# Kernel optimization log

Hardware: AMD Instinct MI355X
Metric: run time of the kernel (lower is better)

## Reference

```python
import jax, jax.numpy as jnp
import numpy as np
from jax import lax

THRESHOLD = 0.7
OUT = 224  # output size of nn.Upsample(size=(224,224), mode='bilinear', align_corners=True)


def _bilinear(img, xs, ys):
    """align_corners=True bilinear sampling. img: (..., H, W); xs: (oh,), ys: (ow,) float coords."""
    H, W = img.shape[-2], img.shape[-1]
    x0 = jnp.clip(jnp.floor(xs).astype(jnp.int32), 0, H - 1)
    x1 = jnp.clip(x0 + 1, 0, H - 1)
    y0 = jnp.clip(jnp.floor(ys).astype(jnp.int32), 0, W - 1)
    y1 = jnp.clip(y0 + 1, 0, W - 1)
    wx = (xs - x0.astype(xs.dtype))[:, None]  # (oh,1)
    wy = (ys - y0.astype(ys.dtype))[None, :]  # (1,ow)
    top = jnp.take(img, x0, axis=-2)
    bot = jnp.take(img, x1, axis=-2)
    v00 = jnp.take(top, y0, axis=-1)
    v01 = jnp.take(top, y1, axis=-1)
    v10 = jnp.take(bot, y0, axis=-1)
    v11 = jnp.take(bot, y1, axis=-1)
    return (1 - wx) * ((1 - wy) * v00 + wy * v01) + wx * ((1 - wy) * v10 + wy * v11)


def _normalize01(h):
    n = h.shape[0]
    f = h.reshape(n, -1)
    mn = f.min(axis=1, keepdims=True)
    mx = f.max(axis=1, keepdims=True)
    return ((f - mn) / (mx - mn)).reshape(h.shape)


def _largest_cc(mask):
    """8-connected (skimage connectivity=2) largest component via min-label propagation.
    mask: (N,H,W) bool -> (N,H,W) bool, True on the largest connected component."""
    N, H, W = mask.shape
    BIG = H * W  # background sentinel label
    idx = jnp.arange(BIG, dtype=jnp.int32).reshape(1, H, W)
    lab0 = jnp.where(mask, idx, BIG)

    def body(state):
        lab, _ = state
        pooled = lax.reduce_window(lab, jnp.int32(BIG), lax.min, (1, 3, 3), (1, 1, 1), 'SAME')
        new = jnp.where(mask, pooled, BIG)
        return new, jnp.any(new != lab)

    lab, _ = lax.while_loop(lambda s: s[1], body, (lab0, jnp.bool_(True)))

    def counts(l):
        return jnp.zeros(BIG + 1, jnp.int32).at[l.reshape(-1)].add(1)

    c = jax.vmap(counts)(lab)                 # (N, H*W+1); last bin = background
    best = jnp.argmax(c[:, :BIG], axis=1)     # label of largest foreground component
    return lab == best[:, None, None]


def _bbox(lcc):
    N, H, W = lcc.shape
    rows = lcc.any(axis=2)
    cols = lcc.any(axis=1)
    has = rows.any(axis=1)
    xmin = jnp.argmax(rows, axis=1).astype(jnp.int32)
    xmax = (H - 1 - jnp.argmax(rows[:, ::-1], axis=1)).astype(jnp.int32)
    ymin = jnp.argmax(cols, axis=1).astype(jnp.int32)
    ymax = (W - 1 - jnp.argmax(cols[:, ::-1], axis=1)).astype(jnp.int32)
    # fallback to full image if the mask is empty (torch code would crash here)
    xmin = jnp.where(has, xmin, 0)
    ymin = jnp.where(has, ymin, 0)
    xmax = jnp.where(has, xmax, H - 1)
    ymax = jnp.where(has, ymax, W - 1)
    return xmin, xmax, ymin, ymax


def _crop_resize(images, xmin, xmax, ymin, ymax):
    # torch crop is images[i][:, xmin:xmax, ymin:ymax] (exclusive upper), then align_corners resize
    grid = jnp.arange(OUT, dtype=jnp.float32) / (OUT - 1)

    def one(img, a, b, c, d):
        Lx = jnp.maximum(b - a, 1)
        Ly = jnp.maximum(d - c, 1)
        xs = a.astype(jnp.float32) + grid * (Lx - 1).astype(jnp.float32)
        ys = c.astype(jnp.float32) + grid * (Ly - 1).astype(jnp.float32)
        return _bilinear(img, xs, ys)

    return jax.vmap(one)(images, xmin, xmax, ymin, ymax)


def setup_inputs() -> dict:
    key = jax.random.key(0)
    k1, k2 = jax.random.split(key)
    x = jax.random.normal(k1, (64, 3, 224, 224), dtype=jnp.float32)
    features = jax.random.normal(k2, (64, 2048, 7, 7), dtype=jnp.float32)
    return {"x": x, "features": features}


def reference(x, features):
    # distance = normalize01(Lmax(features, axis=1))
    heat = _normalize01(jnp.max(jnp.abs(features), axis=1))       # (N, h, w)
    h, w = heat.shape[1], heat.shape[2]
    grid = jnp.arange(OUT, dtype=jnp.float32) / (OUT - 1)
    out_heatmap = _bilinear(heat, grid * (h - 1), grid * (w - 1))  # (N, 224, 224)
    mask = out_heatmap > THRESHOLD
    lcc = _largest_cc(mask)
    xmin, xmax, ymin, ymax = _bbox(lcc)
    crop = _crop_resize(x, xmin, xmax, ymin, ymax)                 # (N, 3, 224, 224)
    coords = jnp.stack([ymin, xmin, ymax, xmax], axis=1)           # (N, 4), torch coord order
    return crop, out_heatmap, coords
```

## Files before the change

### kernel.cpp

```cpp
#include <hip/hip_runtime.h>
#include <stdint.h>

#define NIMG   64
#define NCH    2048
#define HW7    49
#define OUTW   224
#define NPIX   50176
#define CROP_N 9633792
#define HEAT_OFF  9633792
#define COORD_OFF 12845056
#define THRESH 0.7f

#define MAXR 8
#define RCAP (224*MAXR)
#define NWORDS 784
#define WPAD   788

#define SCRATCH_ULL 52480

__global__ __launch_bounds__(256) void k0_zero(unsigned long long* base) {
    int id = blockIdx.x * 256 + threadIdx.x;
    if (id < SCRATCH_ULL) base[id] = 0ull;
}

__global__ __launch_bounds__(256) void k1_heat(const float* __restrict__ F,
                                               unsigned* __restrict__ heatBins) {
    __shared__ unsigned hU[HW7];
    const int t = threadIdx.x;
    const int b = blockIdx.x;
    const int n = b >> 3, chunk = b & 7;
    if (t < HW7) hU[t] = 0u;
    __syncthreads();
    const float* Fp = F + (size_t)n * 100352 + (size_t)chunk * 12544 + t;
    int pos = t % 49;
#pragma unroll
    for (int r = 0; r < 49; ++r) {
        float v = fabsf(Fp[r * 256]);
        atomicMax(&hU[pos], __float_as_uint(v));
        pos += 11; if (pos >= 49) pos -= 49;
    }
    __syncthreads();
    if (t < HW7) atomicMax(&heatBins[n * HW7 + t], hU[t]);
}

__device__ inline float bilin7(const float* h7, int i, int j) {
#pragma clang fp contract(off)
    float gx = (float)i / 223.0f;
    float gy = (float)j / 223.0f;
    float xs = gx * 6.0f;
    float ys = gy * 6.0f;
    int x0 = (int)floorf(xs); x0 = min(max(x0, 0), 6); int x1 = min(x0 + 1, 6);
    int y0 = (int)floorf(ys); y0 = min(max(y0, 0), 6); int y1 = min(y0 + 1, 6);
    float wx = xs - (float)x0;
    float wy = ys - (float)y0;
    float v00 = h7[x0 * 7 + y0], v01 = h7[x0 * 7 + y1];
    float v10 = h7[x1 * 7 + y0], v11 = h7[x1 * 7 + y1];
    return (1.0f - wx) * ((1.0f - wy) * v00 + wy * v01)
         + wx * ((1.0f - wy) * v10 + wy * v11);
}

__global__ __launch_bounds__(256) void k2_heatmap(const unsigned* __restrict__ heatBins,
                                                  float* __restrict__ heatOut,
                                                  unsigned long long* __restrict__ maskW) {
    __shared__ float raw[HW7];
    __shared__ float h7[HW7];
    __shared__ float s_mn, s_mx;
    const int t = threadIdx.x;
    const int b = blockIdx.x;
    const int n = b >> 3, slice = b & 7;
    if (t < HW7) raw[t] = __uint_as_float(heatBins[n * HW7 + t]);
    __syncthreads();
    if (t == 0) {
        float mn = raw[0], mx = raw[0];
        for (int i = 1; i < HW7; ++i) { float v = raw[i]; mn = fminf(mn, v); mx = fmaxf(mx, v); }
        s_mn = mn; s_mx = mx;
    }
    __syncthreads();
    if (t < HW7) h7[t] = (raw[t] - s_mn) / (s_mx - s_mn);
    __syncthreads();

    const int pbase = slice * 6272;
    for (int k = 0; k < 25; ++k) {
        int pl = k * 256 + t;
        if (pl < 6272) {
            int p = pbase + pl;
            int i = p / 224, j = p % 224;
            float val = bilin7(h7, i, j);
            heatOut[(size_t)n * NPIX + p] = val;
            unsigned long long bal = __ballot(val > THRESH);
            if ((t & 63) == 0) maskW[(size_t)n * WPAD + (p >> 6)] = bal;
        }
    }
}

__device__ inline unsigned uf_find(volatile unsigned* P, unsigned x) {
    while (true) {
        unsigned p = P[x];
        if (p == x) return x;
        unsigned gp = P[p];
        if (gp == p) return p;
        P[x] = gp;
        x = gp;
    }
}

__device__ inline void uf_merge(volatile unsigned* P, unsigned a, unsigned b) {
    while (true) {
        a = uf_find(P, a); b = uf_find(P, b);
        if (a == b) return;
        if (a > b) { unsigned tmp = a; a = b; b = tmp; }
        unsigned old = atomicCAS((unsigned*)&P[b], b, a);
        if (old == b) return;
        b = old;
    }
}

__global__ __launch_bounds__(256) void k3_ccl(const unsigned long long* __restrict__ maskW,
                                              float* __restrict__ coords) {
    __shared__ unsigned long long W[WPAD];
    __shared__ unsigned short runS[RCAP], runE[RCAP];
    __shared__ unsigned char nRuns[224];
    __shared__ unsigned parent[RCAP], cnt[RCAP];
    __shared__ unsigned rmin[RCAP], rmax[RCAP], cmin[RCAP], cmax[RCAP];
    __shared__ unsigned bestScore, bestRid;
    const int t = threadIdx.x;
    const int n = blockIdx.x;

    for (int i = t; i < WPAD; i += 256) W[i] = maskW[(size_t)n * WPAD + i];
    for (int i = t; i < RCAP; i += 256) {
        parent[i] = (unsigned)i; cnt[i] = 0u;
        rmin[i] = 0xFFFFFFFFu; rmax[i] = 0u; cmin[i] = 0xFFFFFFFFu; cmax[i] = 0u;
    }
    if (t == 0) { bestScore = 0u; bestRid = 0u; }
    __syncthreads();

    if (t < 224) {
        const int r = t;
        const int bit0 = r * 224;
        const int w0 = bit0 >> 6, sh = bit0 & 63;
        unsigned long long rb[4];
#pragma unroll
        for (int q = 0; q < 4; ++q) {
            unsigned long long lo = W[w0 + q] >> sh;
            unsigned long long hi = sh ? (W[w0 + q + 1] << (64 - sh)) : 0ull;
            rb[q] = lo | hi;
        }
        rb[3] &= 0xFFFFFFFFull;

        unsigned long long st[4], en[4];
        unsigned long long carry = 0ull;
#pragma unroll
        for (int q = 0; q < 4; ++q) {
            unsigned long long shl = (rb[q] << 1) | carry;
            carry = rb[q] >> 63;
            st[q] = rb[q] & ~shl;
        }
#pragma unroll
        for (int q = 0; q < 4; ++q) {
            unsigned long long nxt = (q < 3) ? rb[q + 1] : 0ull;
            en[q] = rb[q] & ~((rb[q] >> 1) | (nxt << 63));
        }
        int ns = 0;
#pragma unroll
        for (int q = 0; q < 4; ++q) {
            unsigned long long x = st[q];
            while (x) {
                int z = __builtin_ctzll(x); x &= x - 1;
                if (ns < MAXR) runS[r * MAXR + ns] = (unsigned short)(q * 64 + z);
                ns++;
            }
        }
        int ne = 0;
#pragma unroll
        for (int q = 0; q < 4; ++q) {
            unsigned long long x = en[q];
            while (x) {
                int z = __builtin_ctzll(x); x &= x - 1;
                if (ne < MAXR) runE[r * MAXR + ne] = (unsigned short)(q * 64 + z);
                ne++;
            }
        }
        nRuns[r] = (unsigned char)min(ns, MAXR);
    }
    __syncthreads();

    if (t >= 1 && t < 224) {
        const int r = t;
        const int na = nRuns[r], nb = nRuns[r - 1];
        for (int k = 0; k < na; ++k) {
            int rid = r * MAXR + k;
            int s = runS[rid], e = runE[rid];
            for (int m = 0; m < nb; ++m) {
                int qid = (r - 1) * MAXR + m;
                int s2 = runS[qid], e2 = runE[qid];
                if (s2 <= e + 1 && e2 >= s - 1) uf_merge(parent, (unsigned)rid, (unsigned)qid);
            }
        }
    }
    __syncthreads();

    for (int rid = t; rid < RCAP; rid += 256) {
        int r = rid >> 3, k = rid & (MAXR - 1);
        if (k < (int)nRuns[r]) {
            int s = runS[rid], e = runE[rid];
            unsigned root = uf_find(parent, (unsigned)rid);
            atomicAdd(&cnt[root], (unsigned)(e - s + 1));
            atomicMin(&rmin[root], (unsigned)r);
            atomicMax(&rmax[root], (unsigned)r);
            atomicMin(&cmin[root], (unsigned)s);
            atomicMax(&cmax[root], (unsigned)e);
        }
    }
    __syncthreads();

    for (int rid = t; rid < RCAP; rid += 256) {
        unsigned c = cnt[rid];
        if (c > 0u) {
            unsigned label = (unsigned)((rid >> 3) * 224 + (int)runS[rid]);
            unsigned score = (c << 16) | (65535u - label);
            atomicMax(&bestScore, score);
        }
    }
    __syncthreads();
    for (int rid = t; rid < RCAP; rid += 256) {
        unsigned c = cnt[rid];
        if (c > 0u) {
            unsigned label = (unsigned)((rid >> 3) * 224 + (int)runS[rid]);
            unsigned score = (c << 16) | (65535u - label);
            if (score == bestScore) bestRid = (unsigned)rid;
        }
    }
    __syncthreads();

    if (t == 0) {
        int xmin, xmax, ymin, ymax;
        if (bestScore == 0u) {
            xmin = 0; ymin = 0; xmax = 223; ymax = 223;
        } else {
            unsigned rb_ = bestRid;
            xmin = (int)rmin[rb_]; xmax = (int)rmax[rb_];
            ymin = (int)cmin[rb_]; ymax = (int)cmax[rb_];
        }
        coords[n * 4 + 0] = (float)ymin;
        coords[n * 4 + 1] = (float)xmin;
        coords[n * 4 + 2] = (float)ymax;
        coords[n * 4 + 3] = (float)xmax;
    }
}

__global__ __launch_bounds__(256) void k4_crop(const float* __restrict__ X,
                                               const float* __restrict__ coords,
                                               float* __restrict__ out) {
#pragma clang fp contract(off)
    int id = blockIdx.x * 256 + threadIdx.x;
    if (id >= CROP_N) return;
    int n   = id / 150528;
    int rem = id % 150528;
    int p   = rem % NPIX;
    int oi  = p / 224, oj = p % 224;

    int ymin = (int)coords[n * 4 + 0];
    int xmin = (int)coords[n * 4 + 1];
    int ymax = (int)coords[n * 4 + 2];
    int xmax = (int)coords[n * 4 + 3];
    int Lx = max(xmax - xmin, 1);
    int Ly = max(ymax - ymin, 1);

    float gx = (float)oi / 223.0f;
    float gy = (float)oj / 223.0f;
    float xs = (float)xmin + gx * (float)(Lx - 1);
    float ys = (float)ymin + gy * (float)(Ly - 1);
    int x0 = (int)floorf(xs); x0 = min(max(x0, 0), 223); int x1 = min(x0 + 1, 223);
    int y0 = (int)floorf(ys); y0 = min(max(y0, 0), 223); int y1 = min(y0 + 1, 223);
    float wx = xs - (float)x0;
    float wy = ys - (float)y0;

    const float* img = X + (size_t)n * 150528 + (size_t)(rem / NPIX) * NPIX;
    float v00 = img[x0 * 224 + y0], v01 = img[x0 * 224 + y1];
    float v10 = img[x1 * 224 + y0], v11 = img[x1 * 224 + y1];
    out[id] = (1.0f - wx) * ((1.0f - wy) * v00 + wy * v01)
            + wx * ((1.0f - wy) * v10 + wy * v11);
}

extern "C" void kernel_launch(void* const* d_in, const int* in_sizes, int n_in,
                              void* d_out, int out_size, void* d_ws, size_t ws_size,
                              hipStream_t stream) {
    (void)in_sizes; (void)n_in; (void)out_size; (void)d_ws; (void)ws_size;
    const float* X = (const float*)d_in[0];
    const float* F = (const float*)d_in[1];
    float* out = (float*)d_out;

    unsigned* heatBins = (unsigned*)d_out;
    unsigned long long* maskW = (unsigned long long*)((char*)d_out + 16384);
    float* heatOut = out + HEAT_OFF;
    float* coords  = out + COORD_OFF;

    k0_zero   <<<dim3((SCRATCH_ULL + 255) / 256), dim3(256), 0, stream>>>((unsigned long long*)d_out);
    k1_heat   <<<dim3(512), dim3(256), 0, stream>>>(F, heatBins);
    k2_heatmap<<<dim3(512), dim3(256), 0, stream>>>(heatBins, heatOut, maskW);
    k3_ccl    <<<dim3(64),  dim3(256), 0, stream>>>(maskW, coords);
    k4_crop   <<<dim3(CROP_N / 256), dim3(256), 0, stream>>>(X, coords, out);
}
```

Measured before the change: 166.0 us.

## Drop zero kernel, use partial-max heat reduction, process three channels per crop thread

Removes the scratch-zeroing kernel by having the heat kernel write per-block partial maxima with plain register reductions instead of shared and global atomics, and the heatmap kernel combines the eight partials. The crop kernel now handles all three channels per thread, so the coordinate and weight arithmetic is shared across channels and a third as many blocks are launched. The CCL kernel zero-pads its mask tail in shared memory instead of reading it from the workspace. Together these cut one launch and the atomic contention, at the cost of a different scratch layout inside the output buffer.

```diff
diff --git a/kernel.cpp b/kernel.cpp
--- a/kernel.cpp
+++ b/kernel.cpp
@@ -16,31 +16,28 @@
 #define NWORDS 784
 #define WPAD   788
 
-#define SCRATCH_ULL 52480
-
-__global__ __launch_bounds__(256) void k0_zero(unsigned long long* base) {
-    int id = blockIdx.x * 256 + threadIdx.x;
-    if (id < SCRATCH_ULL) base[id] = 0ull;
-}
+#define MASKW_BYTE_OFF 131072
 
 __global__ __launch_bounds__(256) void k1_heat(const float* __restrict__ F,
-                                               unsigned* __restrict__ heatBins) {
-    __shared__ unsigned hU[HW7];
+                                               float* __restrict__ heatPart) {
+    __shared__ float smax[4][64];
     const int t = threadIdx.x;
     const int b = blockIdx.x;
-    const int n = b >> 3, chunk = b & 7;
-    if (t < HW7) hU[t] = 0u;
-    __syncthreads();
-    const float* Fp = F + (size_t)n * 100352 + (size_t)chunk * 12544 + t;
-    int pos = t % 49;
-#pragma unroll
-    for (int r = 0; r < 49; ++r) {
-        float v = fabsf(Fp[r * 256]);
-        atomicMax(&hU[pos], __float_as_uint(v));
-        pos += 11; if (pos >= 49) pos -= 49;
-    }
-    __syncthreads();
-    if (t < HW7) atomicMax(&heatBins[n * HW7 + t], hU[t]);
+    const int n = b >> 3, g = b & 7;
+    const int w = t >> 6, l = t & 63;
+    const int lp = (l < HW7) ? l : 0;
+    const float* base = F + (size_t)n * 100352 + (size_t)(g * 256 + w) * HW7 + lp;
+    float vmax = 0.0f;
+#pragma unroll 8
+    for (int i = 0; i < 64; ++i) {
+        vmax = fmaxf(vmax, fabsf(base[(size_t)i * 4 * HW7]));
+    }
+    smax[w][l] = vmax;
+    __syncthreads();
+    if (t < HW7) {
+        float m = fmaxf(fmaxf(smax[0][t], smax[1][t]), fmaxf(smax[2][t], smax[3][t]));
+        heatPart[b * HW7 + t] = m;
+    }
 }
 
 __device__ inline float bilin7(const float* h7, int i, int j) {
@@ -59,7 +56,7 @@
          + wx * ((1.0f - wy) * v10 + wy * v11);
 }
 
-__global__ __launch_bounds__(256) void k2_heatmap(const unsigned* __restrict__ heatBins,
+__global__ __launch_bounds__(256) void k2_heatmap(const float* __restrict__ heatPart,
                                                   float* __restrict__ heatOut,
                                                   unsigned long long* __restrict__ maskW) {
     __shared__ float raw[HW7];
@@ -68,7 +65,12 @@
     const int t = threadIdx.x;
     const int b = blockIdx.x;
     const int n = b >> 3, slice = b & 7;
-    if (t < HW7) raw[t] = __uint_as_float(heatBins[n * HW7 + t]);
+    if (t < HW7) {
+        float m = heatPart[(n * 8 + 0) * HW7 + t];
+#pragma unroll
+        for (int g = 1; g < 8; ++g) m = fmaxf(m, heatPart[(n * 8 + g) * HW7 + t]);
+        raw[t] = m;
+    }
     __syncthreads();
     if (t == 0) {
         float mn = raw[0], mx = raw[0];
@@ -80,6 +82,7 @@
     __syncthreads();
 
     const int pbase = slice * 6272;
+#pragma unroll
     for (int k = 0; k < 25; ++k) {
         int pl = k * 256 + t;
         if (pl < 6272) {
@@ -126,7 +129,8 @@
     const int t = threadIdx.x;
     const int n = blockIdx.x;
 
-    for (int i = t; i < WPAD; i += 256) W[i] = maskW[(size_t)n * WPAD + i];
+    for (int i = t; i < NWORDS; i += 256) W[i] = maskW[(size_t)n * WPAD + i];
+    if (t < WPAD - NWORDS) W[NWORDS + t] = 0ull;
     for (int i = t; i < RCAP; i += 256) {
         parent[i] = (unsigned)i; cnt[i] = 0u;
         rmin[i] = 0xFFFFFFFFu; rmax[i] = 0u; cmin[i] = 0xFFFFFFFFu; cmax[i] = 0u;
@@ -252,12 +256,11 @@
                                                const float* __restrict__ coords,
                                                float* __restrict__ out) {
 #pragma clang fp contract(off)
-    int id = blockIdx.x * 256 + threadIdx.x;
-    if (id >= CROP_N) return;
-    int n   = id / 150528;
-    int rem = id % 150528;
-    int p   = rem % NPIX;
-    int oi  = p / 224, oj = p % 224;
+    const int t = threadIdx.x;
+    const int b = blockIdx.x;
+    const int n = b / 196;
+    const int p = (b % 196) * 256 + t;
+    const int oi = p / 224, oj = p % 224;
 
     int ymin = (int)coords[n * 4 + 0];
     int xmin = (int)coords[n * 4 + 1];
@@ -275,11 +278,19 @@
     float wx = xs - (float)x0;
     float wy = ys - (float)y0;
 
-    const float* img = X + (size_t)n * 150528 + (size_t)(rem / NPIX) * NPIX;
-    float v00 = img[x0 * 224 + y0], v01 = img[x0 * 224 + y1];
-    float v10 = img[x1 * 224 + y0], v11 = img[x1 * 224 + y1];
-    out[id] = (1.0f - wx) * ((1.0f - wy) * v00 + wy * v01)
-            + wx * ((1.0f - wy) * v10 + wy * v11);
+    const float* img = X + (size_t)n * 150528;
+    const size_t o = (size_t)n * 150528 + (size_t)p;
+    const int i00 = x0 * 224 + y0, i01 = x0 * 224 + y1;
+    const int i10 = x1 * 224 + y0, i11 = x1 * 224 + y1;
+#pragma unroll
+    for (int ch = 0; ch < 3; ++ch) {
+        const float* im = img + ch * NPIX;
+        float v00 = im[i00], v01 = im[i01];
+        float v10 = im[i10], v11 = im[i11];
+        out[o + (size_t)ch * NPIX] =
+            (1.0f - wx) * ((1.0f - wy) * v00 + wy * v01)
+          + wx * ((1.0f - wy) * v10 + wy * v11);
+    }
 }
 
 extern "C" void kernel_launch(void* const* d_in, const int* in_sizes, int n_in,
@@ -290,14 +301,13 @@
     const float* F = (const float*)d_in[1];
     float* out = (float*)d_out;
 
-    unsigned* heatBins = (unsigned*)d_out;
-    unsigned long long* maskW = (unsigned long long*)((char*)d_out + 16384);
+    float* heatPart = (float*)d_out;
+    unsigned long long* maskW = (unsigned long long*)((char*)d_out + MASKW_BYTE_OFF);
     float* heatOut = out + HEAT_OFF;
     float* coords  = out + COORD_OFF;
 
-    k0_zero   <<<dim3((SCRATCH_ULL + 255) / 256), dim3(256), 0, stream>>>((unsigned long long*)d_out);
-    k1_heat   <<<dim3(512), dim3(256), 0, stream>>>(F, heatBins);
-    k2_heatmap<<<dim3(512), dim3(256), 0, stream>>>(heatBins, heatOut, maskW);
-    k3_ccl    <<<dim3(64),  dim3(256), 0, stream>>>(maskW, coords);
-    k4_crop   <<<dim3(CROP_N / 256), dim3(256), 0, stream>>>(X, coords, out);
-}
+    k1_heat   <<<dim3(512),   dim3(256), 0, stream>>>(F, heatPart);
+    k2_heatmap<<<dim3(512),   dim3(256), 0, stream>>>(heatPart, heatOut, maskW);
+    k3_ccl    <<<dim3(64),    dim3(256), 0, stream>>>(maskW, coords);
+    k4_crop   <<<dim3(12544), dim3(256), 0, stream>>>(X, coords, out);
+}
```

New measurement: 148.0 us. 10.8% less time.
